# Kernel tuning notes

Hardware: AMD Instinct MI355X
Metric: run time of the kernel (lower is better)

## Reference

```python
import jax, jax.numpy as jnp
import numpy as np

QMIN, QMAX = -128, 127

def make_accurate_lut():
    # lut[i, j] = signed8(j) * signed8(i) with indices taken as uint8 bit patterns
    v = np.arange(256)
    v[v >= 128] -= 256
    xx, yy = np.meshgrid(v, v)
    return jnp.asarray((xx * yy).astype(np.int32))

def setup_inputs() -> dict:
    key = jax.random.key(0)
    kx, kw = jax.random.split(key)
    B, N, M, K = 4, 512, 512, 256
    x = jax.random.normal(kx, (B, N, M), dtype=jnp.float32)
    w = jax.random.normal(kw, (K, M), dtype=jnp.float32)
    return {
        "x": x,
        "w": w,
        "lut": make_accurate_lut(),                       # [256,256] int32
        "x_scale": jnp.ones((1,), jnp.float32) * 0.03,    # per-tensor affine quant params
        "x_zero_point": jnp.zeros((1,), jnp.float32),
        "w_scale": jnp.ones((1,), jnp.float32) * 0.03,
        "w_zero_point": jnp.zeros((1,), jnp.float32),
    }

def _quantize(t, scale, zp):
    # affine quantize to signed int8 range, kept in int32 for indexing
    q = jnp.round(t / scale + zp)
    return jnp.clip(q, QMIN, QMAX).astype(jnp.int32)

def _lut_gemm(xq, wq, lut):
    # xq: [B,N,M] int32 in [-128,127]; wq: [K,M]; lut: [256,256]
    xi = jnp.mod(xq, 256)  # uint8 bit-pattern index
    wi = jnp.mod(wq, 256)
    # gather per-element products via the LUT, then accumulate over M
    prods = lut[xi[:, :, None, :], wi[None, None, :, :]]  # [B,N,K,M] int32
    return prods.sum(axis=-1)                             # [B,N,K] int32

def reference(x, w, lut, x_scale, x_zero_point, w_scale, w_zero_point):
    xs, xzp = x_scale.reshape(()), x_zero_point.reshape(())
    ws, wzp = w_scale.reshape(()), w_zero_point.reshape(())
    M = x.shape[-1]
    xq = _quantize(x, xs, xzp)           # [B,N,M]
    wq = _quantize(w, ws, wzp)           # [K,M]
    acc = _lut_gemm(xq, wq, lut).astype(jnp.float32)  # ~ sum_m xq*wq via LUT
    # affine zero-point correction: sum (xq-xzp)(wq-wzp)
    acc = (acc
           - wzp * jnp.sum(xq, axis=-1, keepdims=True).astype(jnp.float32)
           - xzp * jnp.sum(wq, axis=-1).astype(jnp.float32)[None, None, :]
           + jnp.float32(M) * xzp * wzp)
    return acc * xs * ws                 # dequantized output [B,N,K]
```

## Files before the change

### kernel.cpp

```cpp
#include <hip/hip_runtime.h>

constexpr int Mdim = 512;
constexpr int Kdim = 256;
constexpr int ROWS = 2048;
constexpr int MW   = Mdim / 4;

constexpr int XQ_OFF   = 0;
constexpr int WQ_OFF   = ROWS * MW;
constexpr int XSUM_OFF = WQ_OFF + Kdim * MW;
constexpr int WSUM_OFF = XSUM_OFF + ROWS;

typedef int v4i __attribute__((ext_vector_type(4)));

__device__ __forceinline__ int qz(float v, float scale, float zp) {
    float q = rintf(v / scale + zp);
    q = fminf(fmaxf(q, -128.0f), 127.0f);
    return (int)q;
}

__device__ __forceinline__ int pack4(int q0, int q1, int q2, int q3) {
    return (q0 & 255) | ((q1 & 255) << 8) | ((q2 & 255) << 16) | ((q3 & 255) << 24);
}

__global__ __launch_bounds__(64) void quant_kernel(
        const float* __restrict__ x, const float* __restrict__ w,
        const float* __restrict__ x_scale, const float* __restrict__ x_zp,
        const float* __restrict__ w_scale, const float* __restrict__ w_zp,
        int* __restrict__ ws) {
    const int tid = threadIdx.x;
    const bool is_x = (blockIdx.x < ROWS);
    const int row = is_x ? blockIdx.x : (blockIdx.x - ROWS);
    const float s  = is_x ? x_scale[0] : w_scale[0];
    const float zp = is_x ? x_zp[0]    : w_zp[0];
    const float* src = (is_x ? x : w) + (size_t)row * Mdim;

    const float4* src4 = (const float4*)src;
    float4 a = src4[tid * 2];
    float4 b = src4[tid * 2 + 1];

    int q0 = qz(a.x, s, zp), q1 = qz(a.y, s, zp), q2 = qz(a.z, s, zp), q3 = qz(a.w, s, zp);
    int q4 = qz(b.x, s, zp), q5 = qz(b.y, s, zp), q6 = qz(b.z, s, zp), q7 = qz(b.w, s, zp);

    const int base = (is_x ? XQ_OFF : WQ_OFF) + row * MW + 2 * tid;
    *(int2*)&ws[base] = make_int2(pack4(q0, q1, q2, q3), pack4(q4, q5, q6, q7));

    int sum = q0 + q1 + q2 + q3 + q4 + q5 + q6 + q7;
    #pragma unroll
    for (int off = 32; off > 0; off >>= 1) sum += __shfl_down(sum, off);
    if (tid == 0) ws[(is_x ? XSUM_OFF : WSUM_OFF) + row] = sum;
}

__global__ __launch_bounds__(64) void mfma_gemm_kernel(
        const int* __restrict__ ws,
        const float* __restrict__ x_scale, const float* __restrict__ x_zp,
        const float* __restrict__ w_scale, const float* __restrict__ w_zp,
        float* __restrict__ out) {
    const int lane  = threadIdx.x;
    const int group = lane >> 4;
    const int lo    = lane & 15;
    const int r0 = (blockIdx.x >> 4) * 16;
    const int c0 = (blockIdx.x & 15) * 16;

    const v4i* xa = (const v4i*)&ws[XQ_OFF + (size_t)(r0 + lo) * MW];
    const v4i* wb = (const v4i*)&ws[WQ_OFF + (size_t)(c0 + lo) * MW];

    v4i a[8], b[8];
    #pragma unroll
    for (int kk = 0; kk < 8; ++kk) {
        a[kk] = xa[kk * 4 + group];
        b[kk] = wb[kk * 4 + group];
    }

    v4i acc = {0, 0, 0, 0};
    #pragma unroll
    for (int kk = 0; kk < 8; ++kk)
        acc = __builtin_amdgcn_mfma_i32_16x16x64_i8(a[kk], b[kk], acc, 0, 0, 0);

    const float xs = x_scale[0], xzpf = x_zp[0];
    const float wsf = w_scale[0], wzpf = w_zp[0];
    const float wsumc = (float)ws[WSUM_OFF + c0 + lo];
    const v4i xs4 = *(const v4i*)&ws[XSUM_OFF + r0 + group * 4];
    const float corr = (float)Mdim * xzpf * wzpf - xzpf * wsumc;
    const float oscale = xs * wsf;

    #pragma unroll
    for (int i = 0; i < 4; ++i) {
        const int row = r0 + group * 4 + i;
        float v = (float)acc[i] - wzpf * (float)xs4[i] + corr;
        out[(size_t)row * Kdim + c0 + lo] = v * oscale;
    }
}

extern "C" void kernel_launch(void* const* d_in, const int* in_sizes, int n_in,
                              void* d_out, int out_size, void* d_ws, size_t ws_size,
                              hipStream_t stream) {
    const float* x       = (const float*)d_in[0];
    const float* w       = (const float*)d_in[1];
    const float* x_scale = (const float*)d_in[3];
    const float* x_zp    = (const float*)d_in[4];
    const float* w_scale = (const float*)d_in[5];
    const float* w_zp    = (const float*)d_in[6];
    float* out = (float*)d_out;
    int* ws = (int*)d_ws;

    quant_kernel<<<ROWS + Kdim, 64, 0, stream>>>(x, w, x_scale, x_zp, w_scale, w_zp, ws);
    mfma_gemm_kernel<<<(ROWS / 16) * (Kdim / 16), 64, 0, stream>>>(
        ws, x_scale, x_zp, w_scale, w_zp, out);
}
```

Before: 72.80 us.

## Fuse quantization into MFMA GEMM and compute row sums with ones-MFMAs

Merges the separate quantize kernel and int8 MFMA GEMM into one kernel that quantizes fp32 x and w tiles on the fly, removing the int8 workspace round trip and one launch. Zero-point row and column sums are computed with extra MFMAs against a ones vector instead of shuffle reductions. Division is replaced by multiplication with a precomputed reciprocal, and four 16x16 tiles are packed per 256-thread block. In exchange, each fp32 x row is re-read and re-quantized by all 16 column tiles and each w row by every row tile, which multiplies global fp32 traffic and quantize ALU work. Reciprocal multiply can also round differently from true division at tie points.

```diff
diff --git a/kernel.cpp b/kernel.cpp
--- a/kernel.cpp
+++ b/kernel.cpp
@@ -3,91 +3,75 @@
 constexpr int Mdim = 512;
 constexpr int Kdim = 256;
 constexpr int ROWS = 2048;
-constexpr int MW   = Mdim / 4;
-
-constexpr int XQ_OFF   = 0;
-constexpr int WQ_OFF   = ROWS * MW;
-constexpr int XSUM_OFF = WQ_OFF + Kdim * MW;
-constexpr int WSUM_OFF = XSUM_OFF + ROWS;
 
 typedef int v4i __attribute__((ext_vector_type(4)));
 
-__device__ __forceinline__ int qz(float v, float scale, float zp) {
-    float q = rintf(v / scale + zp);
+__device__ __forceinline__ int qz(float v, float inv, float zp) {
+    float q = rintf(fmaf(v, inv, zp));
     q = fminf(fmaxf(q, -128.0f), 127.0f);
     return (int)q;
 }
 
-__device__ __forceinline__ int pack4(int q0, int q1, int q2, int q3) {
+__device__ __forceinline__ int qpack4(float4 f, float inv, float zp) {
+    int q0 = qz(f.x, inv, zp), q1 = qz(f.y, inv, zp);
+    int q2 = qz(f.z, inv, zp), q3 = qz(f.w, inv, zp);
     return (q0 & 255) | ((q1 & 255) << 8) | ((q2 & 255) << 16) | ((q3 & 255) << 24);
 }
 
-__global__ __launch_bounds__(64) void quant_kernel(
+__device__ __forceinline__ v4i quant16(const float* __restrict__ p, float inv, float zp) {
+    const float4* p4 = (const float4*)p;
+    float4 f0 = p4[0], f1 = p4[1], f2 = p4[2], f3 = p4[3];
+    v4i r;
+    r[0] = qpack4(f0, inv, zp);
+    r[1] = qpack4(f1, inv, zp);
+    r[2] = qpack4(f2, inv, zp);
+    r[3] = qpack4(f3, inv, zp);
+    return r;
+}
+
+__global__ __launch_bounds__(256) void fused_lutgemm_kernel(
         const float* __restrict__ x, const float* __restrict__ w,
         const float* __restrict__ x_scale, const float* __restrict__ x_zp,
         const float* __restrict__ w_scale, const float* __restrict__ w_zp,
-        int* __restrict__ ws) {
-    const int tid = threadIdx.x;
-    const bool is_x = (blockIdx.x < ROWS);
-    const int row = is_x ? blockIdx.x : (blockIdx.x - ROWS);
-    const float s  = is_x ? x_scale[0] : w_scale[0];
-    const float zp = is_x ? x_zp[0]    : w_zp[0];
-    const float* src = (is_x ? x : w) + (size_t)row * Mdim;
+        float* __restrict__ out) {
+    const int lane  = threadIdx.x & 63;
+    const int wv    = threadIdx.x >> 6;
+    const int tile  = blockIdx.x * 4 + wv;
+    const int r0    = (tile >> 4) * 16;
+    const int c0    = (tile & 15) * 16;
+    const int lo    = lane & 15;
+    const int group = lane >> 4;
 
-    const float4* src4 = (const float4*)src;
-    float4 a = src4[tid * 2];
-    float4 b = src4[tid * 2 + 1];
+    const float xs  = x_scale[0], xzp = x_zp[0];
+    const float wsf = w_scale[0], wzp = w_zp[0];
+    const float xinv = 1.0f / xs;
+    const float winv = 1.0f / wsf;
 
-    int q0 = qz(a.x, s, zp), q1 = qz(a.y, s, zp), q2 = qz(a.z, s, zp), q3 = qz(a.w, s, zp);
-    int q4 = qz(b.x, s, zp), q5 = qz(b.y, s, zp), q6 = qz(b.z, s, zp), q7 = qz(b.w, s, zp);
+    const float* xrow = x + (size_t)(r0 + lo) * Mdim;
+    const float* wrow = w + (size_t)(c0 + lo) * Mdim;
 
-    const int base = (is_x ? XQ_OFF : WQ_OFF) + row * MW + 2 * tid;
-    *(int2*)&ws[base] = make_int2(pack4(q0, q1, q2, q3), pack4(q4, q5, q6, q7));
+    v4i acc  = {0, 0, 0, 0};
+    v4i accx = {0, 0, 0, 0};
+    v4i accw = {0, 0, 0, 0};
+    const v4i ones = {0x01010101, 0x01010101, 0x01010101, 0x01010101};
 
-    int sum = q0 + q1 + q2 + q3 + q4 + q5 + q6 + q7;
-    #pragma unroll
-    for (int off = 32; off > 0; off >>= 1) sum += __shfl_down(sum, off);
-    if (tid == 0) ws[(is_x ? XSUM_OFF : WSUM_OFF) + row] = sum;
-}
-
-__global__ __launch_bounds__(64) void mfma_gemm_kernel(
-        const int* __restrict__ ws,
-        const float* __restrict__ x_scale, const float* __restrict__ x_zp,
-        const float* __restrict__ w_scale, const float* __restrict__ w_zp,
-        float* __restrict__ out) {
-    const int lane  = threadIdx.x;
-    const int group = lane >> 4;
-    const int lo    = lane & 15;
-    const int r0 = (blockIdx.x >> 4) * 16;
-    const int c0 = (blockIdx.x & 15) * 16;
-
-    const v4i* xa = (const v4i*)&ws[XQ_OFF + (size_t)(r0 + lo) * MW];
-    const v4i* wb = (const v4i*)&ws[WQ_OFF + (size_t)(c0 + lo) * MW];
-
-    v4i a[8], b[8];
     #pragma unroll
     for (int kk = 0; kk < 8; ++kk) {
-        a[kk] = xa[kk * 4 + group];
-        b[kk] = wb[kk * 4 + group];
+        const int off = kk * 64 + group * 16;
+        v4i a = quant16(xrow + off, xinv, xzp);
+        v4i b = quant16(wrow + off, winv, wzp);
+        acc  = __builtin_amdgcn_mfma_i32_16x16x64_i8(a, b,    acc,  0, 0, 0);
+        accx = __builtin_amdgcn_mfma_i32_16x16x64_i8(a, ones, accx, 0, 0, 0);
+        accw = __builtin_amdgcn_mfma_i32_16x16x64_i8(ones, b, accw, 0, 0, 0);
     }
 
-    v4i acc = {0, 0, 0, 0};
-    #pragma unroll
-    for (int kk = 0; kk < 8; ++kk)
-        acc = __builtin_amdgcn_mfma_i32_16x16x64_i8(a[kk], b[kk], acc, 0, 0, 0);
-
-    const float xs = x_scale[0], xzpf = x_zp[0];
-    const float wsf = w_scale[0], wzpf = w_zp[0];
-    const float wsumc = (float)ws[WSUM_OFF + c0 + lo];
-    const v4i xs4 = *(const v4i*)&ws[XSUM_OFF + r0 + group * 4];
-    const float corr = (float)Mdim * xzpf * wzpf - xzpf * wsumc;
-    const float oscale = xs * wsf;
-
+    const float corr = (float)Mdim * xzp * wzp;
+    const float osc  = xs * wsf;
     #pragma unroll
     for (int i = 0; i < 4; ++i) {
         const int row = r0 + group * 4 + i;
-        float v = (float)acc[i] - wzpf * (float)xs4[i] + corr;
-        out[(size_t)row * Kdim + c0 + lo] = v * oscale;
+        float v = (float)acc[i] - wzp * (float)accx[i] - xzp * (float)accw[i] + corr;
+        out[(size_t)row * Kdim + c0 + lo] = v * osc;
     }
 }
 
@@ -101,9 +85,8 @@
     const float* w_scale = (const float*)d_in[5];
     const float* w_zp    = (const float*)d_in[6];
     float* out = (float*)d_out;
-    int* ws = (int*)d_ws;
+    (void)d_ws; (void)ws_size;
 
-    quant_kernel<<<ROWS + Kdim, 64, 0, stream>>>(x, w, x_scale, x_zp, w_scale, w_zp, ws);
-    mfma_gemm_kernel<<<(ROWS / 16) * (Kdim / 16), 64, 0, stream>>>(
-        ws, x_scale, x_zp, w_scale, w_zp, out);
+    fused_lutgemm_kernel<<<(ROWS / 16) * (Kdim / 16) / 4, 256, 0, stream>>>(
+        x, w, x_scale, x_zp, w_scale, w_zp, out);
 }
```

Result: slower. 80.76 us (+10.9%).
